# Kernel optimization log

Hardware: AMD Instinct MI355X
Metric: run time of the kernel (lower is better)

## Reference

```python
import jax, jax.numpy as jnp
import numpy as np

N_NODES = 16
N_EDGES = 64
N_LAYERS = 4


def _gcn(x, src, dst, emask, W, b):
    # PyG GCNConv: add self-loops, symmetric deg^-1/2 normalization, sum-aggregate.
    n = x.shape[0]
    h = x @ W  # [n, d_out]
    deg = jax.ops.segment_sum(emask, dst, num_segments=n) + 1.0  # +1 self-loop
    dinv = jax.lax.rsqrt(deg)
    norm = dinv[src] * dinv[dst] * emask  # masked-out edges get 0 weight
    out = jax.ops.segment_sum(norm[:, None] * h[src], dst, num_segments=n)
    return out + (dinv * dinv)[:, None] * h + b  # self-loop term + bias


def _sag_pool(x, src, dst, emask, w_rel, b_rel, w_root, k):
    # SAGPooling with GraphConv scorer: score = lin_rel(sum_j x_j) + lin_root(x)
    n = x.shape[0]
    agg = jax.ops.segment_sum(emask[:, None] * x[src], dst, num_segments=n)
    score = agg @ w_rel + b_rel + x @ w_root  # [n]
    perm = jnp.argsort(-score)[:k]  # top-k nodes
    x_new = x[perm] * jnp.tanh(score[perm])[:, None]
    kept = jnp.zeros(n, bool).at[perm].set(True)
    pos = jnp.zeros(n, jnp.int32).at[perm].set(jnp.arange(k, dtype=jnp.int32))
    emask_new = emask * kept[src] * kept[dst]  # drop edges touching removed nodes
    return x_new, pos[src], pos[dst], emask_new


def _conv_gnn(x, src, dst, W0, Ws, bs, pWrel, pbrel, pWroot, linW, linb):
    emask = jnp.ones(src.shape[0], x.dtype)
    n = x.shape[0]
    for i in range(N_LAYERS):
        W = W0 if i == 0 else Ws[i - 1]
        x = jax.nn.relu(_gcn(x, src, dst, emask, W, bs[i]))
        k = -(-n // 2)  # ceil(0.5 * n) -- SAGPooling ratio=0.5
        x, src, dst, emask = _sag_pool(x, src, dst, emask, pWrel[i], pbrel[i], pWroot[i], k)
        n = k
    x = x @ linW + linb  # [1, 128]
    return jax.nn.log_softmax(x, axis=1)


def _fc(h, fcW, fcb, lnw, lnb):
    eps = 1e-5
    for i in range(3):
        h = h @ fcW[i] + fcb[i]
        mu = h.mean(-1, keepdims=True)
        var = ((h - mu) ** 2).mean(-1, keepdims=True)
        h = (h - mu) * jax.lax.rsqrt(var + eps) * lnw[i] + lnb[i]
        h = jax.nn.relu(h)
    return h @ fcW[3] + fcb[3]


def setup_inputs() -> dict:
    key = jax.random.key(0)
    ks = iter(jax.random.split(key, 64))

    def rn(shape, s=0.05):
        return jax.random.normal(next(ks), shape, jnp.float32) * s

    def gnn_params(p):
        return {
            p + '_W0': rn((45, 128)), p + '_W': rn((3, 128, 128)),
            p + '_b': jnp.zeros((4, 128), jnp.float32),
            p + '_pWrel': rn((4, 128)), p + '_pbrel': jnp.zeros((4,), jnp.float32),
            p + '_pWroot': rn((4, 128)),
            p + '_linW': rn((128, 128)), p + '_linb': jnp.zeros((128,), jnp.float32),
        }

    inp = {
        'gp_x': rn((N_NODES, 45), 1.0), 'sp_x': rn((N_NODES, 45), 1.0),
        'gp_src': jax.random.randint(next(ks), (N_EDGES,), 0, N_NODES, jnp.int32),
        'gp_dst': jax.random.randint(next(ks), (N_EDGES,), 0, N_NODES, jnp.int32),
        'sp_src': jax.random.randint(next(ks), (N_EDGES,), 0, N_NODES, jnp.int32),
        'sp_dst': jax.random.randint(next(ks), (N_EDGES,), 0, N_NODES, jnp.int32),
        'fcW': rn((4, 256, 256)), 'fcb': jnp.zeros((4, 256), jnp.float32),
        'lnw': jnp.ones((3, 256), jnp.float32), 'lnb': jnp.zeros((3, 256), jnp.float32),
    }
    inp.update(gnn_params('g'))
    inp.update(gnn_params('s'))
    return inp


def reference(gp_x, sp_x, gp_src, gp_dst, sp_src, sp_dst,
              g_W0, g_W, g_b, g_pWrel, g_pbrel, g_pWroot, g_linW, g_linb,
              s_W0, s_W, s_b, s_pWrel, s_pbrel, s_pWroot, s_linW, s_linb,
              fcW, fcb, lnw, lnb):
    out1 = _conv_gnn(gp_x, gp_src, gp_dst, g_W0, g_W, g_b, g_pWrel, g_pbrel, g_pWroot, g_linW, g_linb)
    out2 = _conv_gnn(sp_x, sp_src, sp_dst, s_W0, s_W, s_b, s_pWrel, s_pbrel, s_pWroot, s_linW, s_linb)
    concat = jnp.concatenate((out1.reshape(-1), out2.reshape(-1)))  # [256]
    return _fc(concat, fcW, fcb, lnw, lnb)
```

## Files before the change

kernel.cpp:

```cpp
#include <hip/hip_runtime.h>
#include <math.h>

#define MAGIC 0x5F3759DFu
typedef unsigned int u32;

__device__ __forceinline__ void bar_lds(){
  asm volatile("s_waitcnt lgkmcnt(0)\n\ts_barrier" ::: "memory");
}
__device__ __forceinline__ void bar_full(){
  asm volatile("s_waitcnt vmcnt(0) lgkmcnt(0)\n\ts_barrier" ::: "memory");
}

__device__ inline float wsum(float v){
  #pragma unroll
  for (int o=32;o;o>>=1) v += __shfl_xor(v,o,64);
  return v;
}
__device__ inline float wmax(float v){
  #pragma unroll
  for (int o=32;o;o>>=1) v = fmaxf(v,__shfl_xor(v,o,64));
  return v;
}

__device__ __forceinline__ void stageW(const float* g, float* l, int nfloats,
                                       int wid, int lane){
  const int nch = nfloats>>8;
  for (int c=wid; c<nch; c+=8)
    __builtin_amdgcn_global_load_lds(
      (__attribute__((address_space(1))) u32*)(void*)(g+(c<<8)+(lane<<2)),
      (__attribute__((address_space(3))) u32*)(void*)(l+(c<<8)), 16, 0, 0);
}

__device__ __forceinline__ void pf(const float* p, int nfloats, int tid){
  float4 acc={0.f,0.f,0.f,0.f};
  const int nq=nfloats>>2;
  for (int i=tid;i<nq;i+=512){
    const float4 v=((const float4*)p)[i];
    acc.x+=v.x; acc.y+=v.y; acc.z+=v.z; acc.w+=v.w;
  }
  asm volatile("" :: "v"(acc.x),"v"(acc.y),"v"(acc.z),"v"(acc.w));
}

__global__ __launch_bounds__(512,1) void net_kernel(
    const float* __restrict__ gp_x, const float* __restrict__ sp_x,
    const int* __restrict__ gp_src, const int* __restrict__ gp_dst,
    const int* __restrict__ sp_src, const int* __restrict__ sp_dst,
    const float* __restrict__ g_W0, const float* __restrict__ g_W,
    const float* __restrict__ g_b,  const float* __restrict__ g_pWrel,
    const float* __restrict__ g_pbrel, const float* __restrict__ g_pWroot,
    const float* __restrict__ g_linW, const float* __restrict__ g_linb,
    const float* __restrict__ s_W0, const float* __restrict__ s_W,
    const float* __restrict__ s_b,  const float* __restrict__ s_pWrel,
    const float* __restrict__ s_pbrel, const float* __restrict__ s_pWroot,
    const float* __restrict__ s_linW, const float* __restrict__ s_linb,
    const float* __restrict__ fcW, const float* __restrict__ fcb,
    const float* __restrict__ lnw, const float* __restrict__ lnb,
    float* __restrict__ wsbuf, float* __restrict__ out)
{
  __shared__ float slotA[16384];
  __shared__ float slotB[16384];
  __shared__ float XBx[16][132];
  __shared__ float ZB[16][132];
  __shared__ float PBf[2048];
  __shared__ float wrelL[512], wrootL[512];
  __shared__ float fcin[256], yA[128];
  __shared__ float wpart[16];
  __shared__ int   esrcA[64]; __shared__ float ewA[64];
  __shared__ int   cntA[16], startA[16];
  __shared__ float dinvA[16], tsA[8];
  __shared__ int   permA[8];

  const int lt  = threadIdx.x;
  const int bid = blockIdx.x;
  const int wid = lt>>6, lane = lt&63;

  if (bid >= 6){
    switch(bid){
      case 8:  pf(g_W0,5760,lt);        pf(g_W,32768,lt);      break;
      case 9:  pf(s_W0,5760,lt);        pf(s_W,32768,lt);      break;
      case 6:  pf(g_W+32768,16384,lt);  pf(g_linW,16384,lt);
               pf(g_pWrel,512,lt);      pf(g_pWroot,512,lt);   break;
      case 7:  pf(s_W+32768,16384,lt);  pf(s_linW,16384,lt);
               pf(s_pWrel,512,lt);      pf(s_pWroot,512,lt);   break;
      case 10: pf(fcW,65536,lt);        break;
      case 11: pf(fcW+65536,65536,lt);  break;
      case 12: pf(fcW+131072,65536,lt); break;
      case 13: pf(fcW+196608,65536,lt); break;
      case 14: pf(fcb,1024,lt); pf(lnw,768,lt); pf(lnb,768,lt); break;
      default: break;
    }
    return;
  }

  if (bid >= 2){
    const int L = bid-2;
    const int qfc=(wid<<3)+(lane&7), f0fc=(lane>>3)<<5;
    float4 wr[32];
    #pragma unroll
    for (int t=0;t<32;++t) wr[t]=*(const float4*)(fcW+(L<<16)+(f0fc+t)*256+(qfc<<2));
    const float4 bb=*(const float4*)(fcb+(L<<8)+(qfc<<2));
    float4 lw={0,0,0,0}, lb2={0,0,0,0};
    if (L<3){ lw=*(const float4*)(lnw+(L<<8)+(qfc<<2)); lb2=*(const float4*)(lnb+(L<<8)+(qfc<<2)); }
    if (lt==0){
      if (L==0){
        const u32* f1=(const u32*)(wsbuf+128);
        const u32* f2=(const u32*)(wsbuf+384);
        while (__hip_atomic_load(f1,__ATOMIC_ACQUIRE,__HIP_MEMORY_SCOPE_AGENT)!=MAGIC ||
               __hip_atomic_load(f2,__ATOMIC_ACQUIRE,__HIP_MEMORY_SCOPE_AGENT)!=MAGIC)
          __builtin_amdgcn_s_sleep(1);
      } else {
        const u32* f1=(const u32*)(wsbuf+512+(L-1)*512+256);
        while (__hip_atomic_load(f1,__ATOMIC_ACQUIRE,__HIP_MEMORY_SCOPE_AGENT)!=MAGIC)
          __builtin_amdgcn_s_sleep(1);
      }
    }
    bar_lds();
    if (lt<256){
      const float* src = (L==0) ? (wsbuf + (lt<128 ? lt : 128+lt))
                                : (wsbuf + 512 + (L-1)*512 + lt);
      fcin[lt]=__hip_atomic_load(src,__ATOMIC_RELAXED,__HIP_MEMORY_SCOPE_AGENT);
    }
    bar_lds();
    float4 a={0.f,0.f,0.f,0.f};
    #pragma unroll
    for (int t=0;t<32;++t){
      const float zv=fcin[f0fc+t];
      a.x+=zv*wr[t].x; a.y+=zv*wr[t].y; a.z+=zv*wr[t].z; a.w+=zv*wr[t].w;
    }
    #pragma unroll
    for (int m=8;m<64;m<<=1){
      a.x+=__shfl_xor(a.x,m,64); a.y+=__shfl_xor(a.y,m,64);
      a.z+=__shfl_xor(a.z,m,64); a.w+=__shfl_xor(a.w,m,64);
    }
    if (L==3){
      if (lane<8){
        float4 r; r.x=a.x+bb.x; r.y=a.y+bb.y; r.z=a.z+bb.z; r.w=a.w+bb.w;
        *(float4*)(out+(qfc<<2))=r;
      }
      return;
    }
    const bool act=(lane<8);
    float4 hv={0.f,0.f,0.f,0.f};
    if (act){
      hv.x=a.x+bb.x; hv.y=a.y+bb.y; hv.z=a.z+bb.z; hv.w=a.w+bb.w;
      float s=hv.x+hv.y+hv.z+hv.w;
      float s2=hv.x*hv.x+hv.y*hv.y+hv.z*hv.z+hv.w*hv.w;
      #pragma unroll
      for (int m=1;m<8;m<<=1){ s+=__shfl_xor(s,m,64); s2+=__shfl_xor(s2,m,64); }
      if (lane==0){ wpart[wid]=s; wpart[8+wid]=s2; }
    }
    bar_lds();
    if (act){
      float S=0.f,S2=0.f;
      #pragma unroll
      for (int w2=0;w2<8;++w2){ S+=wpart[w2]; S2+=wpart[8+w2]; }
      const float mu=S*(1.f/256.f);
      const float ri=rsqrtf(S2*(1.f/256.f)-mu*mu+1e-5f);
      float* dst=wsbuf+512+L*512+(qfc<<2);
      __hip_atomic_store(dst+0, fmaxf((hv.x-mu)*ri*lw.x+lb2.x,0.f), __ATOMIC_RELAXED,__HIP_MEMORY_SCOPE_AGENT);
      __hip_atomic_store(dst+1, fmaxf((hv.y-mu)*ri*lw.y+lb2.y,0.f), __ATOMIC_RELAXED,__HIP_MEMORY_SCOPE_AGENT);
      __hip_atomic_store(dst+2, fmaxf((hv.z-mu)*ri*lw.z+lb2.z,0.f), __ATOMIC_RELAXED,__HIP_MEMORY_SCOPE_AGENT);
      __hip_atomic_store(dst+3, fmaxf((hv.w-mu)*ri*lw.w+lb2.w,0.f), __ATOMIC_RELAXED,__HIP_MEMORY_SCOPE_AGENT);
    }
    __threadfence();
    bar_lds();
    if (lt==0) __hip_atomic_store((u32*)(wsbuf+512+L*512+256), MAGIC, __ATOMIC_RELEASE,__HIP_MEMORY_SCOPE_AGENT);
    return;
  }

  const int br = bid;
  const float* x0    = br ? sp_x    : gp_x;
  const int*   srcg  = br ? sp_src  : gp_src;
  const int*   dstg  = br ? sp_dst  : gp_dst;
  const float* W0    = br ? s_W0    : g_W0;
  const float* Wl    = br ? s_W     : g_W;
  const float* bl    = br ? s_b     : g_b;
  const float* wrel  = br ? s_pWrel : g_pWrel;
  const float* brel  = br ? s_pbrel : g_pbrel;
  const float* wroot = br ? s_pWroot: g_pWroot;
  const float* linW  = br ? s_linW  : g_linW;
  const float* linb  = br ? s_linb  : g_linb;
  float* wsOut = wsbuf + br*256;
  u32*   wsFlag = (u32*)(wsbuf + 128 + br*256);

  float xv[4];
  #pragma unroll
  for (int r=0;r<4;++r){
    const int i=lt+(r<<9), v=i>>7, f=i&127;
    xv[r] = (f<45)? x0[v*45+f] : 0.f;
  }
  int es=0, ed=0; float emk=0.f;
  if (lt<64){ es=srcg[lt]; ed=dstg[lt]; emk=1.f; }
  const float4 brelv = *(const float4*)brel;
  asm volatile("" ::: "memory");

  stageW(Wl,        slotA, 16384, wid, lane);
  stageW(Wl+16384,  slotB, 16384, wid, lane);
  stageW(wrel,  wrelL,  512, wid, lane);
  stageW(wroot, wrootL, 512, wid, lane);

  auto build_csr = [&](int n, float tsrc){
    unsigned long long mymask=0ull; int mystart=0, run=0, mycnt=0, mystartnode=0;
    const bool act = (emk!=0.f);
    for (int v=0; v<n; ++v){
      const unsigned long long m = __ballot(act && (ed==v));
      const int pc = __popcll(m);
      if (ed==v){ mymask=m; mystart=run; }
      if (lt==v){ mycnt=pc; mystartnode=run; }
      run += pc;
    }
    const float dinvlane = rsqrtf(1.f+(float)mycnt);
    const float dvs = __shfl(dinvlane, es, 64);
    const float dvd = __shfl(dinvlane, ed, 64);
    if (act){
      const int idx = mystart + __popcll(mymask & ((1ull<<lt)-1ull));
      esrcA[idx]=es; ewA[idx]=dvs*dvd*tsrc;
    }
    if (lt<n){ cntA[lt]=mycnt; startA[lt]=mystartnode; dinvA[lt]=dinvlane; }
  };

  #pragma unroll
  for (int r=0;r<4;++r){
    const int i=lt+(r<<9), v=i>>7, f=i&127;
    XBx[v][f]=xv[r];
  }
  if (lt<64) build_csr(16, 1.f);
  bar_lds();

  #pragma unroll
  for (int layer=0; layer<4; ++layer){
    const int n=16>>layer, k=n>>1;

    if (layer==0){
      if (lt<256){
        const int v=lt>>4, j4=(lt&15)<<2;
        if (j4<48){
          const float dv=dinvA[v], dv2=dv*dv;
          float4 a=*(const float4*)&XBx[v][j4];
          a.x*=dv2; a.y*=dv2; a.z*=dv2; a.w*=dv2;
          const int st=startA[v], cn=cntA[v];
          for (int i=0;i<cn;++i){
            const int s=esrcA[st+i]; const float w=ewA[st+i];
            const float4 xs=*(const float4*)&XBx[s][j4];
            a.x+=w*xs.x; a.y+=w*xs.y; a.z+=w*xs.z; a.w+=w*xs.w;
          }
          *(float4*)&ZB[v][j4]=a;
        }
      }
    } else {
      if (lt < (n<<5)){
        const int v=lt>>5, j4=(lt&31)<<2;
        const int pv=permA[v];
        const float dv=dinvA[v];
        const float sw=dv*dv*tsA[v];
        float4 a=*(const float4*)&XBx[pv][j4];
        a.x*=sw; a.y*=sw; a.z*=sw; a.w*=sw;
        const int st=startA[v], cn=cntA[v];
        for (int i=0;i<cn;++i){
          const int srow=permA[esrcA[st+i]]; const float w=ewA[st+i];
          const float4 xs=*(const float4*)&XBx[srow][j4];
          a.x+=w*xs.x; a.y+=w*xs.y; a.z+=w*xs.z; a.w+=w*xs.w;
        }
        *(float4*)&ZB[v][j4]=a;
      }
    }
    if (layer==3) bar_full();
    else          bar_lds();

    if (layer==0){
      const int v=lt>>5, j4=(lt&31)<<2;
      const float* zrow=&ZB[v][0];
      const float4 b4=*(const float4*)(bl+j4);
      float4 a={0.f,0.f,0.f,0.f};
      #pragma unroll
      for (int bb=0;bb<2;++bb){
        float4 wr[16]; float zr[16];
        #pragma unroll
        for (int t=0;t<16;++t){ wr[t]=*(const float4*)(W0+(bb*16+t)*128+j4); zr[t]=zrow[bb*16+t]; }
        #pragma unroll
        for (int t=0;t<16;++t){ a.x+=zr[t]*wr[t].x; a.y+=zr[t]*wr[t].y; a.z+=zr[t]*wr[t].z; a.w+=zr[t]*wr[t].w; }
      }
      { float4 wr[13]; float zr[13];
        #pragma unroll
        for (int t=0;t<13;++t){ wr[t]=*(const float4*)(W0+(32+t)*128+j4); zr[t]=zrow[32+t]; }
        #pragma unroll
        for (int t=0;t<13;++t){ a.x+=zr[t]*wr[t].x; a.y+=zr[t]*wr[t].y; a.z+=zr[t]*wr[t].z; a.w+=zr[t]*wr[t].w; }
      }
      XBx[v][j4+0]=fmaxf(a.x+b4.x,0.f);
      XBx[v][j4+1]=fmaxf(a.y+b4.y,0.f);
      XBx[v][j4+2]=fmaxf(a.z+b4.z,0.f);
      XBx[v][j4+3]=fmaxf(a.w+b4.w,0.f);
      bar_full();
    } else {
      const float* slot=(layer&1)?slotA:slotB;
      const int sh=9-layer, nq=512>>layer, S=1<<layer, chunk=128>>layer;
      const int q=lt&(nq-1), fh=lt>>sh;
      const int v=q>>5, j4=(q&31)<<2;
      const float* zrow=&ZB[v][0];
      const int f0=fh*chunk;
      float4 a={0.f,0.f,0.f,0.f};
      #pragma unroll
      for (int f=0; f<chunk; ++f){
        const float zv=zrow[f0+f];
        const float4 w4=*(const float4*)&slot[(f0+f)*128+j4];
        a.x+=zv*w4.x; a.y+=zv*w4.y; a.z+=zv*w4.z; a.w+=zv*w4.w;
      }
      *(float4*)&PBf[lt<<2]=a;
      bar_lds();
      if (lt<nq){
        float4 acc=*(const float4*)(bl+layer*128+((lt&31)<<2));
        #pragma unroll
        for (int f2=0; f2<S; ++f2){
          const float4 p=*(const float4*)&PBf[(f2*nq+lt)<<2];
          acc.x+=p.x; acc.y+=p.y; acc.z+=p.z; acc.w+=p.w;
        }
        const int vv=lt>>5, jj4=(lt&31)<<2;
        XBx[vv][jj4+0]=fmaxf(acc.x,0.f);
        XBx[vv][jj4+1]=fmaxf(acc.y,0.f);
        XBx[vv][jj4+2]=fmaxf(acc.z,0.f);
        XBx[vv][jj4+3]=fmaxf(acc.w,0.f);
      }
      bar_lds();
    }

    if (layer==1) stageW(Wl+32768, slotA, 16384, wid, lane);
    if (layer==2) stageW(linW,     slotB, 16384, wid, lane);
    if (lt<64){
      const int lpsh=2+layer, lpn=1<<lpsh, cf4=8>>layer;
      const int v=lt>>lpsh, part=lt&(lpn-1);
      const int f04=part*cf4;
      float p1=0.f,p2=0.f;
      #pragma unroll
      for (int i=0;i<cf4;++i){
        const float4 xw=*(const float4*)&XBx[v][(f04+i)<<2];
        const float4 w4=*(const float4*)&wrelL[layer*128+((f04+i)<<2)];
        const float4 o4=*(const float4*)&wrootL[layer*128+((f04+i)<<2)];
        p1+=xw.x*w4.x+xw.y*w4.y+xw.z*w4.z+xw.w*w4.w;
        p2+=xw.x*o4.x+xw.y*o4.y+xw.z*o4.z+xw.w*o4.w;
      }
      #pragma unroll
      for (int m=1;m<32;m<<=1) if (m<lpn){ p1+=__shfl_xor(p1,m,64); p2+=__shfl_xor(p2,m,64); }
      float sc=-INFINITY;
      if (lt<n){
        const float bv = (layer==0)?brelv.x:(layer==1)?brelv.y:(layer==2)?brelv.z:brelv.w;
        sc=__shfl(p2, lt<<lpsh, 64) + bv;
        const int st=startA[lt], cn=cntA[lt];
        for (int i=0;i<cn;++i) sc += __shfl(p1, esrcA[st+i]<<lpsh, 64);
      }
      int rank=0;
      for (int u=0;u<n;++u){
        const float su=__shfl(sc,u,64);
        rank += (su>sc || (su==sc && u<lt)) ? 1:0;
      }
      const int kept=(lt<n && rank<k)?1:0;
      const int pos=kept?rank:0;
      const float tval = kept? tanhf(sc) : 0.f;
      if (kept){ permA[rank]=lt; tsA[rank]=tval; }
      const float ts_src = __shfl(tval, es, 64);
      const int ks=__shfl(kept,es,64), kd=__shfl(kept,ed,64);
      const int ps=__shfl(pos,es,64),  pd=__shfl(pos,ed,64);
      emk *= (float)(ks&kd);
      es=ps; ed=pd;
      if (layer<3) build_csr(k, ts_src);
    }
    bar_lds();
  }

  {
    const int oj=(wid<<4)+(lane>>2);
    const int f0=(lane&3)<<5;
    const int prow=permA[0]; const float tsf=tsA[0];
    const float lb=linb[oj];
    float p=0.f;
    #pragma unroll
    for (int f=0; f<32; ++f) p += XBx[prow][f0+f]*slotB[(f0+f)*128+oj];
    p += __shfl_xor(p,1,64); p += __shfl_xor(p,2,64);
    if ((lane&3)==0) yA[oj]=p*tsf+lb;
  }
  bar_lds();
  if (lt<128){
    const int ln=lt&63;
    const float a0=yA[ln], b0=yA[64+ln];
    const float m=wmax(fmaxf(a0,b0));
    const float sum=wsum(expf(a0-m)+expf(b0-m));
    const float lse=m+logf(sum);
    __hip_atomic_store(&wsOut[lt], yA[lt]-lse, __ATOMIC_RELAXED, __HIP_MEMORY_SCOPE_AGENT);
  }
  __threadfence();
  bar_lds();
  if (lt==0) __hip_atomic_store(wsFlag, MAGIC, __ATOMIC_RELEASE, __HIP_MEMORY_SCOPE_AGENT);
}

extern "C" void kernel_launch(void* const* d_in, const int* in_sizes, int n_in,
                              void* d_out, int out_size, void* d_ws, size_t ws_size,
                              hipStream_t stream){
  net_kernel<<<16,512,0,stream>>>(
    (const float*)d_in[0],(const float*)d_in[1],
    (const int*)d_in[2],(const int*)d_in[3],(const int*)d_in[4],(const int*)d_in[5],
    (const float*)d_in[10],(const float*)d_in[11],(const float*)d_in[12],(const float*)d_in[13],
    (const float*)d_in[14],(const float*)d_in[15],(const float*)d_in[16],(const float*)d_in[17],
    (const float*)d_in[18],(const float*)d_in[19],(const float*)d_in[20],(const float*)d_in[21],
    (const float*)d_in[22],(const float*)d_in[23],(const float*)d_in[24],(const float*)d_in[25],
    (const float*)d_in[6],(const float*)d_in[7],(const float*)d_in[8],(const float*)d_in[9],
    (float*)d_ws,(float*)d_out);
}
```

Measured before the change: 26.48 us.

## Fuse first FC layer into GNN branches and switch to dense adjacency aggregation

```diff
diff --git a/kernel.cpp b/kernel.cpp
--- a/kernel.cpp
+++ b/kernel.cpp
@@ -10,7 +10,6 @@
 __device__ __forceinline__ void bar_full(){
   asm volatile("s_waitcnt vmcnt(0) lgkmcnt(0)\n\ts_barrier" ::: "memory");
 }
-
 __device__ inline float wsum(float v){
   #pragma unroll
   for (int o=32;o;o>>=1) v += __shfl_xor(v,o,64);
@@ -21,7 +20,11 @@
   for (int o=32;o;o>>=1) v = fmaxf(v,__shfl_xor(v,o,64));
   return v;
 }
-
+__device__ inline float hsum32(float v){
+  #pragma unroll
+  for (int o=16;o;o>>=1) v += __shfl_xor(v,o,64);
+  return v;
+}
 __device__ __forceinline__ void stageW(const float* g, float* l, int nfloats,
                                        int wid, int lane){
   const int nch = nfloats>>8;
@@ -30,7 +33,6 @@
       (__attribute__((address_space(1))) u32*)(void*)(g+(c<<8)+(lane<<2)),
       (__attribute__((address_space(3))) u32*)(void*)(l+(c<<8)), 16, 0, 0);
 }
-
 __device__ __forceinline__ void pf(const float* p, int nfloats, int tid){
   float4 acc={0.f,0.f,0.f,0.f};
   const int nq=nfloats>>2;
@@ -57,43 +59,40 @@
     const float* __restrict__ lnw, const float* __restrict__ lnb,
     float* __restrict__ wsbuf, float* __restrict__ out)
 {
-  __shared__ float slotA[16384];
-  __shared__ float slotB[16384];
-  __shared__ float XBx[16][132];
-  __shared__ float ZB[16][132];
-  __shared__ float PBf[2048];
-  __shared__ float wrelL[512], wrootL[512];
-  __shared__ float fcin[256], yA[128];
+  __shared__ __align__(16) float slotA[16384];
+  __shared__ __align__(16) float XBx[16][128];
+  __shared__ __align__(16) float ZB[8][128];
+  __shared__ __align__(16) float PBf[5120];
+  __shared__ __align__(16) float wrelL[512];
+  __shared__ __align__(16) float wrootL[512];
+  __shared__ __align__(16) float Adn[256];
+  __shared__ __align__(16) float Mdn[256];
+  __shared__ float d1P[32], d2P[32];
   __shared__ float wpart[16];
-  __shared__ int   esrcA[64]; __shared__ float ewA[64];
-  __shared__ int   cntA[16], startA[16];
-  __shared__ float dinvA[16], tsA[8];
+  __shared__ float tsA[8];
   __shared__ int   permA[8];
 
   const int lt  = threadIdx.x;
   const int bid = blockIdx.x;
   const int wid = lt>>6, lane = lt&63;
-
-  if (bid >= 6){
+  float* const fcin = &PBf[4608];
+  float* const yA   = &PBf[4864];
+
+  if (bid >= 5){
     switch(bid){
-      case 8:  pf(g_W0,5760,lt);        pf(g_W,32768,lt);      break;
-      case 9:  pf(s_W0,5760,lt);        pf(s_W,32768,lt);      break;
-      case 6:  pf(g_W+32768,16384,lt);  pf(g_linW,16384,lt);
-               pf(g_pWrel,512,lt);      pf(g_pWroot,512,lt);   break;
-      case 7:  pf(s_W+32768,16384,lt);  pf(s_linW,16384,lt);
-               pf(s_pWrel,512,lt);      pf(s_pWroot,512,lt);   break;
-      case 10: pf(fcW,65536,lt);        break;
-      case 11: pf(fcW+65536,65536,lt);  break;
-      case 12: pf(fcW+131072,65536,lt); break;
-      case 13: pf(fcW+196608,65536,lt); break;
-      case 14: pf(fcb,1024,lt); pf(lnw,768,lt); pf(lnb,768,lt); break;
+      case 5: pf(g_linW,16384,lt); break;
+      case 6: pf(s_linW,16384,lt); break;
+      case 8: pf(g_W0,5760,lt); pf(g_W,32768,lt); pf(g_W+32768,16384,lt);
+              pf(fcW,32768,lt); break;
+      case 9: pf(s_W0,5760,lt); pf(s_W,32768,lt); pf(s_W+32768,16384,lt);
+              pf(fcW+32768,32768,lt); break;
       default: break;
     }
     return;
   }
 
   if (bid >= 2){
-    const int L = bid-2;
+    const int L = bid-1;
     const int qfc=(wid<<3)+(lane&7), f0fc=(lane>>3)<<5;
     float4 wr[32];
     #pragma unroll
@@ -101,26 +100,45 @@
     const float4 bb=*(const float4*)(fcb+(L<<8)+(qfc<<2));
     float4 lw={0,0,0,0}, lb2={0,0,0,0};
     if (L<3){ lw=*(const float4*)(lnw+(L<<8)+(qfc<<2)); lb2=*(const float4*)(lnb+(L<<8)+(qfc<<2)); }
-    if (lt==0){
-      if (L==0){
-        const u32* f1=(const u32*)(wsbuf+128);
-        const u32* f2=(const u32*)(wsbuf+384);
+    float b0=0.f,w0=0.f,l0=0.f;
+    if (bid==2 && lt<256){ b0=fcb[lt]; w0=lnw[lt]; l0=lnb[lt]; }
+
+    if (bid==2){
+      if (lt==0){
+        const u32* f1=(const u32*)(wsbuf+256);
+        const u32* f2=(const u32*)(wsbuf+576);
         while (__hip_atomic_load(f1,__ATOMIC_ACQUIRE,__HIP_MEMORY_SCOPE_AGENT)!=MAGIC ||
                __hip_atomic_load(f2,__ATOMIC_ACQUIRE,__HIP_MEMORY_SCOPE_AGENT)!=MAGIC)
           __builtin_amdgcn_s_sleep(1);
-      } else {
-        const u32* f1=(const u32*)(wsbuf+512+(L-1)*512+256);
+      }
+      bar_lds();
+      float h=0.f;
+      if (lt<256){
+        h = __hip_atomic_load(wsbuf+lt,    __ATOMIC_RELAXED,__HIP_MEMORY_SCOPE_AGENT)
+          + __hip_atomic_load(wsbuf+320+lt,__ATOMIC_RELAXED,__HIP_MEMORY_SCOPE_AGENT) + b0;
+        float s=wsum(h), s2=wsum(h*h);
+        if (lane==0){ wpart[wid]=s; wpart[8+wid]=s2; }
+      }
+      bar_lds();
+      if (lt<256){
+        const float S =wpart[0]+wpart[1]+wpart[2]+wpart[3];
+        const float S2=wpart[8]+wpart[9]+wpart[10]+wpart[11];
+        const float mu=S*(1.f/256.f);
+        const float ri=rsqrtf(S2*(1.f/256.f)-mu*mu+1e-5f);
+        fcin[lt]=fmaxf((h-mu)*ri*w0+l0,0.f);
+      }
+      bar_lds();
+    } else {
+      const int src=(bid==3)?640:960, fl=(bid==3)?896:1216;
+      if (lt==0){
+        const u32* f1=(const u32*)(wsbuf+fl);
         while (__hip_atomic_load(f1,__ATOMIC_ACQUIRE,__HIP_MEMORY_SCOPE_AGENT)!=MAGIC)
           __builtin_amdgcn_s_sleep(1);
       }
-    }
-    bar_lds();
-    if (lt<256){
-      const float* src = (L==0) ? (wsbuf + (lt<128 ? lt : 128+lt))
-                                : (wsbuf + 512 + (L-1)*512 + lt);
-      fcin[lt]=__hip_atomic_load(src,__ATOMIC_RELAXED,__HIP_MEMORY_SCOPE_AGENT);
-    }
-    bar_lds();
+      bar_lds();
+      if (lt<256) fcin[lt]=__hip_atomic_load(wsbuf+src+lt,__ATOMIC_RELAXED,__HIP_MEMORY_SCOPE_AGENT);
+      bar_lds();
+    }
     float4 a={0.f,0.f,0.f,0.f};
     #pragma unroll
     for (int t=0;t<32;++t){
@@ -132,7 +150,7 @@
       a.x+=__shfl_xor(a.x,m,64); a.y+=__shfl_xor(a.y,m,64);
       a.z+=__shfl_xor(a.z,m,64); a.w+=__shfl_xor(a.w,m,64);
     }
-    if (L==3){
+    if (bid==4){
       if (lane<8){
         float4 r; r.x=a.x+bb.x; r.y=a.y+bb.y; r.z=a.z+bb.z; r.w=a.w+bb.w;
         *(float4*)(out+(qfc<<2))=r;
@@ -156,15 +174,15 @@
       for (int w2=0;w2<8;++w2){ S+=wpart[w2]; S2+=wpart[8+w2]; }
       const float mu=S*(1.f/256.f);
       const float ri=rsqrtf(S2*(1.f/256.f)-mu*mu+1e-5f);
-      float* dst=wsbuf+512+L*512+(qfc<<2);
-      __hip_atomic_store(dst+0, fmaxf((hv.x-mu)*ri*lw.x+lb2.x,0.f), __ATOMIC_RELAXED,__HIP_MEMORY_SCOPE_AGENT);
-      __hip_atomic_store(dst+1, fmaxf((hv.y-mu)*ri*lw.y+lb2.y,0.f), __ATOMIC_RELAXED,__HIP_MEMORY_SCOPE_AGENT);
-      __hip_atomic_store(dst+2, fmaxf((hv.z-mu)*ri*lw.z+lb2.z,0.f), __ATOMIC_RELAXED,__HIP_MEMORY_SCOPE_AGENT);
-      __hip_atomic_store(dst+3, fmaxf((hv.w-mu)*ri*lw.w+lb2.w,0.f), __ATOMIC_RELAXED,__HIP_MEMORY_SCOPE_AGENT);
+      float* dst=wsbuf + ((bid==2)?640:960) + (qfc<<2);
+      __hip_atomic_store(dst+0,fmaxf((hv.x-mu)*ri*lw.x+lb2.x,0.f),__ATOMIC_RELAXED,__HIP_MEMORY_SCOPE_AGENT);
+      __hip_atomic_store(dst+1,fmaxf((hv.y-mu)*ri*lw.y+lb2.y,0.f),__ATOMIC_RELAXED,__HIP_MEMORY_SCOPE_AGENT);
+      __hip_atomic_store(dst+2,fmaxf((hv.z-mu)*ri*lw.z+lb2.z,0.f),__ATOMIC_RELAXED,__HIP_MEMORY_SCOPE_AGENT);
+      __hip_atomic_store(dst+3,fmaxf((hv.w-mu)*ri*lw.w+lb2.w,0.f),__ATOMIC_RELAXED,__HIP_MEMORY_SCOPE_AGENT);
     }
     __threadfence();
     bar_lds();
-    if (lt==0) __hip_atomic_store((u32*)(wsbuf+512+L*512+256), MAGIC, __ATOMIC_RELEASE,__HIP_MEMORY_SCOPE_AGENT);
+    if (lt==0) __hip_atomic_store((u32*)(wsbuf+((bid==2)?896:1216)),MAGIC,__ATOMIC_RELEASE,__HIP_MEMORY_SCOPE_AGENT);
     return;
   }
 
@@ -178,10 +196,10 @@
   const float* wrel  = br ? s_pWrel : g_pWrel;
   const float* brel  = br ? s_pbrel : g_pbrel;
   const float* wroot = br ? s_pWroot: g_pWroot;
-  const float* linW  = br ? s_linW  : g_linW;
+  const float* linWg = br ? s_linW  : g_linW;
   const float* linb  = br ? s_linb  : g_linb;
-  float* wsOut = wsbuf + br*256;
-  u32*   wsFlag = (u32*)(wsbuf + 128 + br*256);
+  float* wsOut = wsbuf + (br?320:0);
+  u32*   wsFlag = (u32*)(wsbuf + (br?576:256));
 
   float xv[4];
   #pragma unroll
@@ -192,160 +210,44 @@
   int es=0, ed=0; float emk=0.f;
   if (lt<64){ es=srcg[lt]; ed=dstg[lt]; emk=1.f; }
   const float4 brelv = *(const float4*)brel;
+  float4 blv[4];
+  #pragma unroll
+  for (int L=0;L<4;++L) blv[L]=*(const float4*)(bl + L*128 + ((lt&31)<<2));
+  const float linb_s = (lt<128)? linb[lt] : 0.f;
   asm volatile("" ::: "memory");
-
-  stageW(Wl,        slotA, 16384, wid, lane);
-  stageW(Wl+16384,  slotB, 16384, wid, lane);
   stageW(wrel,  wrelL,  512, wid, lane);
   stageW(wroot, wrootL, 512, wid, lane);
 
-  auto build_csr = [&](int n, float tsrc){
-    unsigned long long mymask=0ull; int mystart=0, run=0, mycnt=0, mystartnode=0;
-    const bool act = (emk!=0.f);
-    for (int v=0; v<n; ++v){
-      const unsigned long long m = __ballot(act && (ed==v));
-      const int pc = __popcll(m);
-      if (ed==v){ mymask=m; mystart=run; }
-      if (lt==v){ mycnt=pc; mystartnode=run; }
-      run += pc;
-    }
-    const float dinvlane = rsqrtf(1.f+(float)mycnt);
-    const float dvs = __shfl(dinvlane, es, 64);
-    const float dvd = __shfl(dinvlane, ed, 64);
+  auto build_dense = [&](int kk, float wlane, bool with_ts){
+    const float4 z4={0.f,0.f,0.f,0.f};
+    *(float4*)&Adn[lt<<2]=z4;
+    *(float4*)&Mdn[lt<<2]=z4;
+    const bool act=(emk!=0.f);
+    int mycnt=0;
+    for (int v=0;v<kk;++v){
+      const unsigned long long m=__ballot(act && (ed==v));
+      if (lt==v) mycnt=__popcll(m);
+    }
+    const float dinvlane=rsqrtf(1.f+(float)mycnt);
+    const float dvs=__shfl(dinvlane,es,64);
+    const float dvd=__shfl(dinvlane,ed,64);
     if (act){
-      const int idx = mystart + __popcll(mymask & ((1ull<<lt)-1ull));
-      esrcA[idx]=es; ewA[idx]=dvs*dvd*tsrc;
-    }
-    if (lt<n){ cntA[lt]=mycnt; startA[lt]=mystartnode; dinvA[lt]=dinvlane; }
+      atomicAdd(&Adn[ed*16+es], dvs*dvd*wlane);
+      atomicAdd(&Mdn[ed*16+es], 1.f);
+    }
+    if (lt<kk){
+      const float tv = with_ts ? tsA[lt] : 1.f;
+      atomicAdd(&Adn[lt*17], dinvlane*dinvlane*tv);
+    }
   };
-
-  #pragma unroll
-  for (int r=0;r<4;++r){
-    const int i=lt+(r<<9), v=i>>7, f=i&127;
-    XBx[v][f]=xv[r];
-  }
-  if (lt<64) build_csr(16, 1.f);
-  bar_lds();
-
-  #pragma unroll
-  for (int layer=0; layer<4; ++layer){
-    const int n=16>>layer, k=n>>1;
-
-    if (layer==0){
-      if (lt<256){
-        const int v=lt>>4, j4=(lt&15)<<2;
-        if (j4<48){
-          const float dv=dinvA[v], dv2=dv*dv;
-          float4 a=*(const float4*)&XBx[v][j4];
-          a.x*=dv2; a.y*=dv2; a.z*=dv2; a.w*=dv2;
-          const int st=startA[v], cn=cntA[v];
-          for (int i=0;i<cn;++i){
-            const int s=esrcA[st+i]; const float w=ewA[st+i];
-            const float4 xs=*(const float4*)&XBx[s][j4];
-            a.x+=w*xs.x; a.y+=w*xs.y; a.z+=w*xs.z; a.w+=w*xs.w;
-          }
-          *(float4*)&ZB[v][j4]=a;
-        }
-      }
-    } else {
-      if (lt < (n<<5)){
-        const int v=lt>>5, j4=(lt&31)<<2;
-        const int pv=permA[v];
-        const float dv=dinvA[v];
-        const float sw=dv*dv*tsA[v];
-        float4 a=*(const float4*)&XBx[pv][j4];
-        a.x*=sw; a.y*=sw; a.z*=sw; a.w*=sw;
-        const int st=startA[v], cn=cntA[v];
-        for (int i=0;i<cn;++i){
-          const int srow=permA[esrcA[st+i]]; const float w=ewA[st+i];
-          const float4 xs=*(const float4*)&XBx[srow][j4];
-          a.x+=w*xs.x; a.y+=w*xs.y; a.z+=w*xs.z; a.w+=w*xs.w;
-        }
-        *(float4*)&ZB[v][j4]=a;
-      }
-    }
-    if (layer==3) bar_full();
-    else          bar_lds();
-
-    if (layer==0){
-      const int v=lt>>5, j4=(lt&31)<<2;
-      const float* zrow=&ZB[v][0];
-      const float4 b4=*(const float4*)(bl+j4);
-      float4 a={0.f,0.f,0.f,0.f};
-      #pragma unroll
-      for (int bb=0;bb<2;++bb){
-        float4 wr[16]; float zr[16];
-        #pragma unroll
-        for (int t=0;t<16;++t){ wr[t]=*(const float4*)(W0+(bb*16+t)*128+j4); zr[t]=zrow[bb*16+t]; }
-        #pragma unroll
-        for (int t=0;t<16;++t){ a.x+=zr[t]*wr[t].x; a.y+=zr[t]*wr[t].y; a.z+=zr[t]*wr[t].z; a.w+=zr[t]*wr[t].w; }
-      }
-      { float4 wr[13]; float zr[13];
-        #pragma unroll
-        for (int t=0;t<13;++t){ wr[t]=*(const float4*)(W0+(32+t)*128+j4); zr[t]=zrow[32+t]; }
-        #pragma unroll
-        for (int t=0;t<13;++t){ a.x+=zr[t]*wr[t].x; a.y+=zr[t]*wr[t].y; a.z+=zr[t]*wr[t].z; a.w+=zr[t]*wr[t].w; }
-      }
-      XBx[v][j4+0]=fmaxf(a.x+b4.x,0.f);
-      XBx[v][j4+1]=fmaxf(a.y+b4.y,0.f);
-      XBx[v][j4+2]=fmaxf(a.z+b4.z,0.f);
-      XBx[v][j4+3]=fmaxf(a.w+b4.w,0.f);
-      bar_full();
-    } else {
-      const float* slot=(layer&1)?slotA:slotB;
-      const int sh=9-layer, nq=512>>layer, S=1<<layer, chunk=128>>layer;
-      const int q=lt&(nq-1), fh=lt>>sh;
-      const int v=q>>5, j4=(q&31)<<2;
-      const float* zrow=&ZB[v][0];
-      const int f0=fh*chunk;
-      float4 a={0.f,0.f,0.f,0.f};
-      #pragma unroll
-      for (int f=0; f<chunk; ++f){
-        const float zv=zrow[f0+f];
-        const float4 w4=*(const float4*)&slot[(f0+f)*128+j4];
-        a.x+=zv*w4.x; a.y+=zv*w4.y; a.z+=zv*w4.z; a.w+=zv*w4.w;
-      }
-      *(float4*)&PBf[lt<<2]=a;
-      bar_lds();
-      if (lt<nq){
-        float4 acc=*(const float4*)(bl+layer*128+((lt&31)<<2));
-        #pragma unroll
-        for (int f2=0; f2<S; ++f2){
-          const float4 p=*(const float4*)&PBf[(f2*nq+lt)<<2];
-          acc.x+=p.x; acc.y+=p.y; acc.z+=p.z; acc.w+=p.w;
-        }
-        const int vv=lt>>5, jj4=(lt&31)<<2;
-        XBx[vv][jj4+0]=fmaxf(acc.x,0.f);
-        XBx[vv][jj4+1]=fmaxf(acc.y,0.f);
-        XBx[vv][jj4+2]=fmaxf(acc.z,0.f);
-        XBx[vv][jj4+3]=fmaxf(acc.w,0.f);
-      }
-      bar_lds();
-    }
-
-    if (layer==1) stageW(Wl+32768, slotA, 16384, wid, lane);
-    if (layer==2) stageW(linW,     slotB, 16384, wid, lane);
+  auto do_E = [&](int n, int k, float bv, bool rebuild){
     if (lt<64){
-      const int lpsh=2+layer, lpn=1<<lpsh, cf4=8>>layer;
-      const int v=lt>>lpsh, part=lt&(lpn-1);
-      const int f04=part*cf4;
-      float p1=0.f,p2=0.f;
-      #pragma unroll
-      for (int i=0;i<cf4;++i){
-        const float4 xw=*(const float4*)&XBx[v][(f04+i)<<2];
-        const float4 w4=*(const float4*)&wrelL[layer*128+((f04+i)<<2)];
-        const float4 o4=*(const float4*)&wrootL[layer*128+((f04+i)<<2)];
-        p1+=xw.x*w4.x+xw.y*w4.y+xw.z*w4.z+xw.w*w4.w;
-        p2+=xw.x*o4.x+xw.y*o4.y+xw.z*o4.z+xw.w*o4.w;
-      }
-      #pragma unroll
-      for (int m=1;m<32;m<<=1) if (m<lpn){ p1+=__shfl_xor(p1,m,64); p2+=__shfl_xor(p2,m,64); }
       float sc=-INFINITY;
       if (lt<n){
-        const float bv = (layer==0)?brelv.x:(layer==1)?brelv.y:(layer==2)?brelv.z:brelv.w;
-        sc=__shfl(p2, lt<<lpsh, 64) + bv;
-        const int st=startA[lt], cn=cntA[lt];
-        for (int i=0;i<cn;++i) sc += __shfl(p1, esrcA[st+i]<<lpsh, 64);
+        float acc=d2P[2*lt]+d2P[2*lt+1]+bv;
+        for (int u=0;u<n;++u)
+          acc += Mdn[lt*16+u]*(d1P[2*u]+d1P[2*u+1]);
+        sc=acc;
       }
       int rank=0;
       for (int u=0;u<n;++u){
@@ -354,28 +256,170 @@
       }
       const int kept=(lt<n && rank<k)?1:0;
       const int pos=kept?rank:0;
-      const float tval = kept? tanhf(sc) : 0.f;
+      const float tval=kept?tanhf(sc):0.f;
       if (kept){ permA[rank]=lt; tsA[rank]=tval; }
-      const float ts_src = __shfl(tval, es, 64);
+      const float ts_src=__shfl(tval,es,64);
       const int ks=__shfl(kept,es,64), kd=__shfl(kept,ed,64);
       const int ps=__shfl(pos,es,64),  pd=__shfl(pos,ed,64);
       emk *= (float)(ks&kd);
       es=ps; ed=pd;
-      if (layer<3) build_csr(k, ts_src);
-    }
-    bar_lds();
-  }
+      if (rebuild) build_dense(k, ts_src, true);
+    }
+  };
+  auto do_B = [&](int n){
+    if (lt < (n<<5)){
+      const int v=lt>>5, j4=(lt&31)<<2;
+      float4 a={0.f,0.f,0.f,0.f};
+      for (int u=0;u<n;++u){
+        const float w=Adn[v*16+u];
+        const float4 xs=*(const float4*)&XBx[permA[u]][j4];
+        a.x+=w*xs.x; a.y+=w*xs.y; a.z+=w*xs.z; a.w+=w*xs.w;
+      }
+      *(float4*)&ZB[v][j4]=a;
+    }
+  };
+  auto cmain = [&](const float* Wb, int nact, int R){
+    if (lt<nact){
+      const int c4=lt&31, s=(lt>>5)&3, f0=s<<5;
+      const int r0=(nact==256)? ((lt>>7)<<2) : 0;
+      float4 a0={0,0,0,0},a1=a0,a2=a0,a3=a0;
+      for (int bb=0;bb<4;++bb){
+        float4 wq[8];
+        #pragma unroll
+        for (int t=0;t<8;++t) wq[t]=*(const float4*)&Wb[(f0+(bb<<3)+t)*128+(c4<<2)];
+        #pragma unroll
+        for (int t=0;t<8;++t){
+          const int f=f0+(bb<<3)+t;
+          const float z0=ZB[r0+0][f], z1=ZB[r0+1][f];
+          a0.x+=z0*wq[t].x; a0.y+=z0*wq[t].y; a0.z+=z0*wq[t].z; a0.w+=z0*wq[t].w;
+          a1.x+=z1*wq[t].x; a1.y+=z1*wq[t].y; a1.z+=z1*wq[t].z; a1.w+=z1*wq[t].w;
+          if (R==4){
+            const float z2=ZB[r0+2][f], z3=ZB[r0+3][f];
+            a2.x+=z2*wq[t].x; a2.y+=z2*wq[t].y; a2.z+=z2*wq[t].z; a2.w+=z2*wq[t].w;
+            a3.x+=z3*wq[t].x; a3.y+=z3*wq[t].y; a3.z+=z3*wq[t].z; a3.w+=z3*wq[t].w;
+          }
+        }
+      }
+      float4* P4=(float4*)PBf;
+      const int pb=lt*5;
+      P4[pb]=a0; P4[pb+1]=a1;
+      if (R==4){ P4[pb+2]=a2; P4[pb+3]=a3; }
+    }
+  };
+  auto creduce = [&](int layer, int n, float4 bl4){
+    if (lt < (n<<5)){
+      const int v=lt>>5, c4=lt&31;
+      const int base=(n==8)? ((v>>2)<<7) : 0;
+      const int row =(n==8)? (v&3) : v;
+      float4 acc=bl4;
+      #pragma unroll
+      for (int s=0;s<4;++s){
+        const float4 p=((const float4*)PBf)[(base+(s<<5)+c4)*5+row];
+        acc.x+=p.x; acc.y+=p.y; acc.z+=p.z; acc.w+=p.w;
+      }
+      float4 o;
+      o.x=fmaxf(acc.x,0.f); o.y=fmaxf(acc.y,0.f);
+      o.z=fmaxf(acc.z,0.f); o.w=fmaxf(acc.w,0.f);
+      *(float4*)&XBx[v][c4<<2]=o;
+      const float4 wr4=*(const float4*)&wrelL[(layer<<7)+(c4<<2)];
+      const float4 wo4=*(const float4*)&wrootL[(layer<<7)+(c4<<2)];
+      float p1=o.x*wr4.x+o.y*wr4.y+o.z*wr4.z+o.w*wr4.w;
+      float p2=o.x*wo4.x+o.y*wo4.y+o.z*wo4.z+o.w*wo4.w;
+      p1=hsum32(p1); p2=hsum32(p2);
+      if ((lane&31)==0){ d1P[2*v]=p1; d1P[2*v+1]=0.f; d2P[2*v]=p2; d2P[2*v+1]=0.f; }
+    }
+  };
+
+  #pragma unroll
+  for (int r=0;r<4;++r){
+    const int i=lt+(r<<9), v=i>>7, f=i&127;
+    XBx[v][f]=xv[r];
+  }
+  if (lt<64) build_dense(16, 1.f, false);
+  bar_lds();
+
+  if (lt<256){
+    const int v=lt>>4, j4=(lt&15)<<2;
+    if (j4<48){
+      float4 a={0.f,0.f,0.f,0.f};
+      for (int u=0;u<16;++u){
+        const float w=Adn[v*16+u];
+        const float4 xs=*(const float4*)&XBx[u][j4];
+        a.x+=w*xs.x; a.y+=w*xs.y; a.z+=w*xs.z; a.w+=w*xs.w;
+      }
+      *(float4*)&PBf[v*48+j4]=a;
+    }
+  }
+  bar_full();
 
   {
-    const int oj=(wid<<4)+(lane>>2);
-    const int f0=(lane&3)<<5;
-    const int prow=permA[0]; const float tsf=tsA[0];
-    const float lb=linb[oj];
+    const int v=lt>>5, j4=(lt&31)<<2;
+    const float* zrow=&PBf[v*48];
+    float4 a={0.f,0.f,0.f,0.f};
+    #pragma unroll
+    for (int bb=0;bb<2;++bb){
+      float4 wr[16]; float zr[16];
+      #pragma unroll
+      for (int t=0;t<16;++t){ wr[t]=*(const float4*)(W0+(bb*16+t)*128+j4); zr[t]=zrow[bb*16+t]; }
+      #pragma unroll
+      for (int t=0;t<16;++t){ a.x+=zr[t]*wr[t].x; a.y+=zr[t]*wr[t].y; a.z+=zr[t]*wr[t].z; a.w+=zr[t]*wr[t].w; }
+    }
+    { float4 wr[13]; float zr[13];
+      #pragma unroll
+      for (int t=0;t<13;++t){ wr[t]=*(const float4*)(W0+(32+t)*128+j4); zr[t]=zrow[32+t]; }
+      #pragma unroll
+      for (int t=0;t<13;++t){ a.x+=zr[t]*wr[t].x; a.y+=zr[t]*wr[t].y; a.z+=zr[t]*wr[t].z; a.w+=zr[t]*wr[t].w; }
+    }
+    float4 o;
+    o.x=fmaxf(a.x+blv[0].x,0.f); o.y=fmaxf(a.y+blv[0].y,0.f);
+    o.z=fmaxf(a.z+blv[0].z,0.f); o.w=fmaxf(a.w+blv[0].w,0.f);
+    *(float4*)&XBx[v][j4]=o;
+    const float4 wr4=*(const float4*)&wrelL[j4];
+    const float4 wo4=*(const float4*)&wrootL[j4];
+    float p1=o.x*wr4.x+o.y*wr4.y+o.z*wr4.z+o.w*wr4.w;
+    float p2=o.x*wo4.x+o.y*wo4.y+o.z*wo4.z+o.w*wo4.w;
+    p1=hsum32(p1); p2=hsum32(p2);
+    if ((lane&31)==0){ d1P[2*v]=p1; d1P[2*v+1]=0.f; d2P[2*v]=p2; d2P[2*v+1]=0.f; }
+  }
+  stageW(Wl, slotA, 16384, wid, lane);
+  bar_lds();
+
+  do_E(16, 8, brelv.x, true);  bar_lds();
+  do_B(8);                     bar_full();
+  cmain(slotA, 256, 4);        bar_lds();
+  creduce(1, 8, blv[1]);       bar_lds();
+  do_E(8, 4, brelv.y, true);   bar_lds();
+  do_B(4);                     bar_lds();
+  cmain(Wl+16384, 128, 4);     bar_lds();
+  stageW(Wl+32768, slotA, 16384, wid, lane);
+  creduce(2, 4, blv[2]);       bar_lds();
+  do_E(4, 2, brelv.z, true);   bar_lds();
+  do_B(2);                     bar_full();
+  cmain(slotA, 128, 2);        bar_lds();
+  creduce(3, 2, blv[3]);       bar_lds();
+  do_E(2, 1, brelv.w, false);  bar_lds();
+
+  const int qg=lt&63, fhg=lt>>6;
+  float4 wfc[16];
+  #pragma unroll
+  for (int t=0;t<16;++t)
+    wfc[t]=*(const float4*)(fcW + (br*128 + fhg*16 + t)*256 + (qg<<2));
+
+  {
+    const int oj=lt&127, fh=lt>>7;
+    const int prow=permA[0];
     float p=0.f;
     #pragma unroll
-    for (int f=0; f<32; ++f) p += XBx[prow][f0+f]*slotB[(f0+f)*128+oj];
-    p += __shfl_xor(p,1,64); p += __shfl_xor(p,2,64);
-    if ((lane&3)==0) yA[oj]=p*tsf+lb;
+    for (int i=0;i<32;++i){
+      const int f=(fh<<5)+i;
+      p += XBx[prow][f]*linWg[f*128+oj];
+    }
+    PBf[(fh<<7)+oj]=p;
+  }
+  bar_lds();
+  if (lt<128){
+    const float y=PBf[lt]+PBf[128+lt]+PBf[256+lt]+PBf[384+lt];
+    yA[lt]=y*tsA[0]+linb_s;
   }
   bar_lds();
   if (lt<128){
@@ -384,17 +428,41 @@
     const float m=wmax(fmaxf(a0,b0));
     const float sum=wsum(expf(a0-m)+expf(b0-m));
     const float lse=m+logf(sum);
-    __hip_atomic_store(&wsOut[lt], yA[lt]-lse, __ATOMIC_RELAXED, __HIP_MEMORY_SCOPE_AGENT);
+    fcin[lt]=yA[lt]-lse;
+  }
+  bar_lds();
+  {
+    float4 acc={0.f,0.f,0.f,0.f};
+    #pragma unroll
+    for (int t=0;t<16;++t){
+      const float zv=fcin[fhg*16+t];
+      acc.x+=zv*wfc[t].x; acc.y+=zv*wfc[t].y; acc.z+=zv*wfc[t].z; acc.w+=zv*wfc[t].w;
+    }
+    ((float4*)PBf)[(fhg<<6)+qg]=acc;
+  }
+  bar_lds();
+  if (lt<64){
+    float4 a={0.f,0.f,0.f,0.f};
+    #pragma unroll
+    for (int fh=0;fh<8;++fh){
+      const float4 p=((const float4*)PBf)[(fh<<6)+lt];
+      a.x+=p.x; a.y+=p.y; a.z+=p.z; a.w+=p.w;
+    }
+    float* dst=wsOut+(lt<<2);
+    __hip_atomic_store(dst+0,a.x,__ATOMIC_RELAXED,__HIP_MEMORY_SCOPE_AGENT);
+    __hip_atomic_store(dst+1,a.y,__ATOMIC_RELAXED,__HIP_MEMORY_SCOPE_AGENT);
+    __hip_atomic_store(dst+2,a.z,__ATOMIC_RELAXED,__HIP_MEMORY_SCOPE_AGENT);
+    __hip_atomic_store(dst+3,a.w,__ATOMIC_RELAXED,__HIP_MEMORY_SCOPE_AGENT);
   }
   __threadfence();
   bar_lds();
-  if (lt==0) __hip_atomic_store(wsFlag, MAGIC, __ATOMIC_RELEASE, __HIP_MEMORY_SCOPE_AGENT);
+  if (lt==0) __hip_atomic_store(wsFlag,MAGIC,__ATOMIC_RELEASE,__HIP_MEMORY_SCOPE_AGENT);
 }
 
 extern "C" void kernel_launch(void* const* d_in, const int* in_sizes, int n_in,
                               void* d_out, int out_size, void* d_ws, size_t ws_size,
                               hipStream_t stream){
-  net_kernel<<<16,512,0,stream>>>(
+  net_kernel<<<10,512,0,stream>>>(
     (const float*)d_in[0],(const float*)d_in[1],
     (const int*)d_in[2],(const int*)d_in[3],(const int*)d_in[4],(const int*)d_in[5],
     (const float*)d_in[10],(const float*)d_in[11],(const float*)d_in[12],(const float*)d_in[13],
```

New measurement: 32.80 us. +23.8%, slower.
